# Kernel tuning notes

Measured on AMD Instinct MI355X. Metric: run time of the kernel, lower is better.

The kernel has to match this reference:

```python
import jax, jax.numpy as jnp
import numpy as np

EMBED_DIM = 1024
NUM_HEADS = 16
HEAD_DIM = EMBED_DIM // NUM_HEADS


def setup_inputs() -> dict:
    key = jax.random.key(0)
    k_x, k_wqkv, k_bqkv, k_wout, k_bout = jax.random.split(key, 5)
    scale = 1.0 / np.sqrt(EMBED_DIM)
    return {
        "x": jax.random.normal(k_x, (2, 2048, EMBED_DIM), dtype=jnp.float32),
        "W_qkv": jax.random.normal(k_wqkv, (3 * EMBED_DIM, EMBED_DIM), dtype=jnp.float32) * scale,
        "b_qkv": jax.random.normal(k_bqkv, (3 * EMBED_DIM,), dtype=jnp.float32) * scale,
        "W_out": jax.random.normal(k_wout, (EMBED_DIM, EMBED_DIM), dtype=jnp.float32) * scale,
        "b_out": jax.random.normal(k_bout, (EMBED_DIM,), dtype=jnp.float32) * scale,
    }


def reference(x, W_qkv, b_qkv, W_out, b_out):
    B, L, D = x.shape
    H, hd = NUM_HEADS, HEAD_DIM
    # fused QKV projection (torch Linear: x @ W.T + b)
    qkv = x @ W_qkv.T + b_qkv                      # [B, L, 3D]
    q, k, v = jnp.split(qkv, 3, axis=-1)           # each [B, L, D]
    # [B, L, D] -> [B, H, L, hd]
    q = q.reshape(B, L, H, hd).transpose(0, 2, 1, 3)
    k = k.reshape(B, L, H, hd).transpose(0, 2, 1, 3)
    v = v.reshape(B, L, H, hd).transpose(0, 2, 1, 3)
    attn = jnp.einsum("bhqd,bhkd->bhqk", q, k) / jnp.sqrt(jnp.float32(hd))
    attn = jax.nn.softmax(attn, axis=-1)           # [B, H, L, L]
    out = jnp.einsum("bhqk,bhkd->bhqd", attn, v)   # [B, H, L, hd]
    out = out.transpose(0, 2, 1, 3).reshape(B, L, D)
    return out @ W_out.T + b_out
```

## Files before the change

kernel.cpp:

```cpp
#include <hip/hip_runtime.h>
#include <hip/hip_bf16.h>

typedef __attribute__((ext_vector_type(8))) _Float16 f16x8;
typedef __attribute__((ext_vector_type(4))) _Float16 f16x4;
typedef __attribute__((ext_vector_type(2))) _Float16 f16x2;
typedef __attribute__((ext_vector_type(4))) float f32x4;
typedef __attribute__((ext_vector_type(16))) float f32x16;
typedef __attribute__((ext_vector_type(2))) __fp16 fp16v2;

__device__ __forceinline__ void gload16(const void* g, void* l) {
  __builtin_amdgcn_global_load_lds((const __attribute__((address_space(1))) void*)g,
                                   (__attribute__((address_space(3))) void*)l, 16, 0, 0);
}
__device__ __forceinline__ float fexp2(float x) {
#if __has_builtin(__builtin_amdgcn_exp2f)
  return __builtin_amdgcn_exp2f(x);
#else
  return exp2f(x);
#endif
}
__device__ __forceinline__ unsigned pk2(float a, float b) {
#if __has_builtin(__builtin_amdgcn_cvt_pkrtz)
  fp16v2 r = __builtin_amdgcn_cvt_pkrtz(a, b);
  return __builtin_bit_cast(unsigned, r);
#else
  f16x2 t;
  t[0] = (_Float16)a;
  t[1] = (_Float16)b;
  return __builtin_bit_cast(unsigned, t);
#endif
}

__global__ __launch_bounds__(256) void cast_all(const float* __restrict__ x,
                                                const float* __restrict__ wqkv,
                                                const float* __restrict__ wout,
                                                _Float16* __restrict__ xh,
                                                _Float16* __restrict__ wqkvh,
                                                _Float16* __restrict__ wouth) {
  const int i = (blockIdx.x * 256 + threadIdx.x) * 8;
  const float* s;
  _Float16* d;
  int off;
  if (i < 4194304) {
    s = x; d = xh; off = i;
  } else if (i < 7340032) {
    s = wqkv; d = wqkvh; off = i - 4194304;
  } else {
    s = wout; d = wouth; off = i - 7340032;
  }
  const float4 v0 = *reinterpret_cast<const float4*>(s + off);
  const float4 v1 = *reinterpret_cast<const float4*>(s + off + 4);
  f16x8 h;
  h[0] = (_Float16)v0.x; h[1] = (_Float16)v0.y; h[2] = (_Float16)v0.z; h[3] = (_Float16)v0.w;
  h[4] = (_Float16)v1.x; h[5] = (_Float16)v1.y; h[6] = (_Float16)v1.z; h[7] = (_Float16)v1.w;
  *reinterpret_cast<f16x8*>(d + off) = h;
}

__global__ __launch_bounds__(256) void gemm_qkv(
    const _Float16* __restrict__ A, const _Float16* __restrict__ Bm,
    const float* __restrict__ bias,
    _Float16* __restrict__ Qo, _Float16* __restrict__ Ko, _Float16* __restrict__ Vto,
    int Ndim, int Kdim) {
  __shared__ __align__(16) _Float16 As[2][4096];
  __shared__ __align__(16) _Float16 Bs[2][4096];
  const int tid = threadIdx.x, lane = tid & 63, wave = tid >> 6;
  const int wm = wave >> 1, wn = wave & 1;
  const int nwg = gridDim.x * gridDim.y;
  int bidl = blockIdx.y * gridDim.x + blockIdx.x;
  bidl = (bidl & 7) * (nwg >> 3) + (bidl >> 3);
  const int m0 = (bidl / gridDim.x) * 128, n0 = (bidl % gridDim.x) * 128;
  const int row = lane & 15, kk = (lane >> 4) * 8;

  const int r0 = tid >> 2, c0 = (tid & 3) * 8;
  const int r1 = (256 + tid) >> 2, c1 = ((256 + tid) & 3) * 8;
  const _Float16* a0 = A + (size_t)(m0 + r0) * Kdim + c0;
  const _Float16* a1 = A + (size_t)(m0 + r1) * Kdim + c1;
  const _Float16* b0 = Bm + (size_t)(n0 + r0) * Kdim + c0;
  const _Float16* b1 = Bm + (size_t)(n0 + r1) * Kdim + c1;

  f32x4 acc[4][4];
#pragma unroll
  for (int i = 0; i < 4; ++i)
#pragma unroll
    for (int j = 0; j < 4; ++j)
#pragma unroll
      for (int q = 0; q < 4; ++q) acc[i][j][q] = 0.f;

  auto STAGE = [&](int bufi, int k0) {
    char* dA = (char*)&As[bufi][0] + (wave * 64) * 16;
    char* dB = (char*)&Bs[bufi][0] + (wave * 64) * 16;
    gload16(a0 + k0, dA);
    gload16(a1 + k0, dA + 4096);
    gload16(b0 + k0, dB);
    gload16(b1 + k0, dB + 4096);
  };

  STAGE(0, 0);
  asm volatile("s_waitcnt vmcnt(0)" ::: "memory");
  __syncthreads();

  for (int k0 = 0; k0 < Kdim; k0 += 32) {
    const int cur = (k0 >> 5) & 1;
    if (k0 + 32 < Kdim) STAGE(cur ^ 1, k0 + 32);
    f16x8 af[4], bf[4];
#pragma unroll
    for (int i = 0; i < 4; ++i)
      af[i] = *reinterpret_cast<const f16x8*>(&As[cur][(wm * 64 + i * 16 + row) * 32 + kk]);
#pragma unroll
    for (int j = 0; j < 4; ++j)
      bf[j] = *reinterpret_cast<const f16x8*>(&Bs[cur][(wn * 64 + j * 16 + row) * 32 + kk]);
#pragma unroll
    for (int i = 0; i < 4; ++i)
#pragma unroll
      for (int j = 0; j < 4; ++j)
        acc[i][j] = __builtin_amdgcn_mfma_f32_16x16x32_f16(af[i], bf[j], acc[i][j], 0, 0, 0);
    asm volatile("s_waitcnt vmcnt(0)" ::: "memory");
    __syncthreads();
  }

  const int part = n0 >> 10;
  if (part == 2) {
#pragma unroll
    for (int i = 0; i < 4; ++i) {
      const int gm = m0 + wm * 64 + i * 16 + (lane >> 4) * 4;
      const int b = gm >> 11, l0 = gm & 2047;
#pragma unroll
      for (int j = 0; j < 4; ++j) {
        const int gn = n0 + wn * 64 + j * 16 + row;
        const int dD = gn & 1023;
        const int h = dD >> 6, dd = dD & 63;
        const float bb = bias[gn];
        f16x4 v;
#pragma unroll
        for (int q = 0; q < 4; ++q) v[q] = (_Float16)(acc[i][j][q] + bb);
        *reinterpret_cast<f16x4*>(&Vto[((size_t)(b * 16 + h) * 64 + dd) * 2048 + l0]) = v;
      }
    }
  } else {
#pragma unroll
    for (int i = 0; i < 4; ++i) {
#pragma unroll
      for (int j = 0; j < 4; ++j) {
#pragma unroll
        for (int q = 0; q < 4; ++q) {
          const int gm = m0 + wm * 64 + i * 16 + (lane >> 4) * 4 + q;
          const int gn = n0 + wn * 64 + j * 16 + row;
          const float c = acc[i][j][q] + bias[gn];
          const int b = gm >> 11, l = gm & 2047;
          const int dD = gn & 1023;
          const int h = dD >> 6, dd = dD & 63;
          const int bh = b * 16 + h;
          if (part == 0)
            Qo[((size_t)bh * 2048 + l) * 64 + dd] = (_Float16)(c * 0.1803368801f);
          else
            Ko[((size_t)bh * 2048 + l) * 64 + dd] = (_Float16)c;
        }
      }
    }
  }
}

__global__ __launch_bounds__(256) void gemm_out64(
    const _Float16* __restrict__ A, const _Float16* __restrict__ Bm,
    const float* __restrict__ bias, float* __restrict__ Cout, int Ndim, int Kdim) {
  __shared__ __align__(16) _Float16 As[2][4096];
  __shared__ __align__(16) _Float16 Bs[2][2048];
  const int tid = threadIdx.x, lane = tid & 63, wave = tid >> 6;
  const int wm = wave >> 1, wn = wave & 1;
  const int nwg = gridDim.x * gridDim.y;
  int bidl = blockIdx.y * gridDim.x + blockIdx.x;
  bidl = (bidl & 7) * (nwg >> 3) + (bidl >> 3);
  const int m0 = (bidl / gridDim.x) * 128, n0 = (bidl % gridDim.x) * 64;
  const int row = lane & 15, kk = (lane >> 4) * 8;

  const int r0 = tid >> 2, c0 = (tid & 3) * 8;
  const int r1 = (256 + tid) >> 2, c1 = ((256 + tid) & 3) * 8;
  const _Float16* a0 = A + (size_t)(m0 + r0) * Kdim + c0;
  const _Float16* a1 = A + (size_t)(m0 + r1) * Kdim + c1;
  const _Float16* b0 = Bm + (size_t)(n0 + r0) * Kdim + c0;

  f32x4 acc[4][2];
#pragma unroll
  for (int i = 0; i < 4; ++i)
#pragma unroll
    for (int j = 0; j < 2; ++j)
#pragma unroll
      for (int q = 0; q < 4; ++q) acc[i][j][q] = 0.f;

  auto STAGE = [&](int bufi, int k0) {
    char* dA = (char*)&As[bufi][0] + (wave * 64) * 16;
    char* dB = (char*)&Bs[bufi][0] + wave * 1024;
    gload16(a0 + k0, dA);
    gload16(a1 + k0, dA + 4096);
    gload16(b0 + k0, dB);
  };

  STAGE(0, 0);
  asm volatile("s_waitcnt vmcnt(0)" ::: "memory");
  __syncthreads();

  for (int k0 = 0; k0 < Kdim; k0 += 32) {
    const int cur = (k0 >> 5) & 1;
    if (k0 + 32 < Kdim) STAGE(cur ^ 1, k0 + 32);
    f16x8 af[4], bf[2];
#pragma unroll
    for (int i = 0; i < 4; ++i)
      af[i] = *reinterpret_cast<const f16x8*>(&As[cur][(wm * 64 + i * 16 + row) * 32 + kk]);
#pragma unroll
    for (int j = 0; j < 2; ++j)
      bf[j] = *reinterpret_cast<const f16x8*>(&Bs[cur][(wn * 32 + j * 16 + row) * 32 + kk]);
#pragma unroll
    for (int i = 0; i < 4; ++i)
#pragma unroll
      for (int j = 0; j < 2; ++j)
        acc[i][j] = __builtin_amdgcn_mfma_f32_16x16x32_f16(af[i], bf[j], acc[i][j], 0, 0, 0);
    asm volatile("s_waitcnt vmcnt(0)" ::: "memory");
    __syncthreads();
  }

#pragma unroll
  for (int i = 0; i < 4; ++i) {
#pragma unroll
    for (int j = 0; j < 2; ++j) {
#pragma unroll
      for (int q = 0; q < 4; ++q) {
        const int gm = m0 + wm * 64 + i * 16 + (lane >> 4) * 4 + q;
        const int gn = n0 + wn * 32 + j * 16 + row;
        Cout[(size_t)gm * Ndim + gn] = acc[i][j][q] + bias[gn];
      }
    }
  }
}

__global__ __launch_bounds__(256, 2) void attn_fwd(const _Float16* __restrict__ Qh,
                                                   const _Float16* __restrict__ Kh,
                                                   const _Float16* __restrict__ Vth,
                                                   _Float16* __restrict__ AOh) {
  __shared__ __align__(16) uint4 KVs[2][1024];
  const int tid = threadIdx.x, lane = tid & 63, wave = tid >> 6;
  const int bid = blockIdx.x;
  const int bh = bid & 31, qb = bid >> 5;
  const int b = bh >> 4, h = bh & 15;
  const int q0 = qb * 128 + wave * 32;
  const _Float16* Qp = Qh + ((size_t)bh * 2048 + q0) * 64;
  const _Float16* Kp = Kh + (size_t)bh * 2048 * 64;
  const _Float16* Vp = Vth + (size_t)bh * 64 * 2048;
  const int r31 = lane & 31, hl = lane >> 5, r7 = lane & 7;

  const int kr0 = tid >> 3, ks0 = (tid & 7) ^ (kr0 & 7);
  const int kr1 = (256 + tid) >> 3, ks1 = ((256 + tid) & 7) ^ (kr1 & 7);
  const _Float16* ksrc0 = Kp + (size_t)kr0 * 64 + ks0 * 8;
  const _Float16* ksrc1 = Kp + (size_t)kr1 * 64 + ks1 * 8;
  const _Float16* vsrc0 = Vp + (size_t)kr0 * 2048 + ks0 * 8;
  const _Float16* vsrc1 = Vp + (size_t)kr1 * 2048 + ks1 * 8;

  f16x8 qf[4];
#pragma unroll
  for (int kd = 0; kd < 4; ++kd)
    qf[kd] = *reinterpret_cast<const f16x8*>(&Qp[r31 * 64 + kd * 16 + hl * 8]);

  f32x16 o0, o1;
#pragma unroll
  for (int i = 0; i < 16; ++i) { o0[i] = 0.f; o1[i] = 0.f; }
  float mrun = 0.f, lsum = 0.f;

  auto STAGE = [&](uint4* base, int t) {
    gload16(ksrc0 + (size_t)t * 4096, base + wave * 64);
    gload16(ksrc1 + (size_t)t * 4096, base + 256 + wave * 64);
    gload16(vsrc0 + t * 64, base + 512 + wave * 64);
    gload16(vsrc1 + t * 64, base + 768 + wave * 64);
  };

  auto ITER = [&](int t, uint4* cur, uint4* nxt) {
    if (t < 31) STAGE(nxt, t + 1);
    const char* KB = (const char*)cur;
    const char* VB = (const char*)(cur + 512);

    const float negm = -mrun;
    f32x16 st[2];
    __builtin_amdgcn_s_setprio(1);
#pragma unroll
    for (int t32 = 0; t32 < 2; ++t32) {
#pragma unroll
      for (int i = 0; i < 16; ++i) st[t32][i] = negm;
#pragma unroll
      for (int kd = 0; kd < 4; ++kd) {
        const f16x8 kf = *reinterpret_cast<const f16x8*>(
            KB + (((t32 * 32 + r31) * 8 + ((kd * 2 + hl) ^ r7)) << 4));
        st[t32] = __builtin_amdgcn_mfma_f32_32x32x16_f16(kf, qf[kd], st[t32], 0, 0, 0);
      }
    }
    __builtin_amdgcn_s_setprio(0);

    f16x8 vf[2][2][2];
#pragma unroll
    for (int hh = 0; hh < 2; ++hh)
#pragma unroll
      for (int t32 = 0; t32 < 2; ++t32)
#pragma unroll
        for (int s = 0; s < 2; ++s)
          vf[hh][t32][s] = *reinterpret_cast<const f16x8*>(
              VB + (((hh * 32 + r31) * 8 + (((t32 * 2 + s) * 2 + hl) ^ r7)) << 4));

    float m16[16];
#pragma unroll
    for (int i = 0; i < 16; ++i) m16[i] = fmaxf(st[0][i], st[1][i]);
#pragma unroll
    for (int w = 8; w; w >>= 1)
#pragma unroll
      for (int i = 0; i < 8; ++i)
        if (i < w) m16[i] = fmaxf(m16[i], m16[i + w]);
    const float mt = m16[0];
    if (!__all(mt <= 11.f)) {
      const float mts = fmaxf(mt, __shfl_xor(mt, 32));
      const float d = fmaxf(mts, 0.f);
      const float al = fexp2(-d);
      lsum *= al;
#pragma unroll
      for (int i = 0; i < 16; ++i) { o0[i] *= al; o1[i] *= al; }
      mrun += d;
#pragma unroll
      for (int t32 = 0; t32 < 2; ++t32)
#pragma unroll
        for (int i = 0; i < 16; ++i) st[t32][i] -= d;
    }
    float pr[32];
#pragma unroll
    for (int i = 0; i < 16; ++i) pr[i] = fexp2(st[0][i]);
#pragma unroll
    for (int i = 0; i < 16; ++i) pr[16 + i] = fexp2(st[1][i]);
    float s16[16];
#pragma unroll
    for (int i = 0; i < 16; ++i) s16[i] = pr[i] + pr[16 + i];
#pragma unroll
    for (int w = 8; w; w >>= 1)
#pragma unroll
      for (int i = 0; i < 8; ++i)
        if (i < w) s16[i] += s16[i + w];
    lsum += s16[0];

    __builtin_amdgcn_s_setprio(1);
#pragma unroll
    for (int t32 = 0; t32 < 2; ++t32) {
#pragma unroll
      for (int s = 0; s < 2; ++s) {
        const int bi = t32 * 16 + s * 8;
        const unsigned Aw = pk2(pr[bi + 0], pr[bi + 1]);
        const unsigned A2 = pk2(pr[bi + 2], pr[bi + 3]);
        const unsigned Bw = pk2(pr[bi + 4], pr[bi + 5]);
        const unsigned B2 = pk2(pr[bi + 6], pr[bi + 7]);
        const unsigned r1 = __shfl_xor(hl ? Aw : Bw, 32);
        const unsigned r2 = __shfl_xor(hl ? A2 : B2, 32);
        union { unsigned u[4]; f16x8 v; } pf;
        pf.u[0] = hl ? r1 : Aw;
        pf.u[1] = hl ? r2 : A2;
        pf.u[2] = hl ? Bw : r1;
        pf.u[3] = hl ? B2 : r2;
        o0 = __builtin_amdgcn_mfma_f32_32x32x16_f16(vf[0][t32][s], pf.v, o0, 0, 0, 0);
        o1 = __builtin_amdgcn_mfma_f32_32x32x16_f16(vf[1][t32][s], pf.v, o1, 0, 0, 0);
      }
    }
    __builtin_amdgcn_s_setprio(0);

    if (t < 31) {
      asm volatile("s_waitcnt vmcnt(0)" ::: "memory");
      __syncthreads();
    }
  };

  STAGE(KVs[0], 0);
  asm volatile("s_waitcnt vmcnt(0)" ::: "memory");
  __syncthreads();

  for (int tt = 0; tt < 16; ++tt) {
    ITER(2 * tt, KVs[0], KVs[1]);
    ITER(2 * tt + 1, KVs[1], KVs[0]);
  }

  const float ltot = lsum + __shfl_xor(lsum, 32);
  const float inv = 1.f / ltot;
  const size_t orow = (size_t)b * 2048 + q0 + r31;
#pragma unroll
  for (int hh = 0; hh < 2; ++hh) {
#pragma unroll
    for (int rr = 0; rr < 4; ++rr) {
      f16x4 c;
#pragma unroll
      for (int j = 0; j < 4; ++j)
        c[j] = (_Float16)((hh ? o1[rr * 4 + j] : o0[rr * 4 + j]) * inv);
      const int hd = 8 * rr + 4 * hl + 32 * hh;
      *reinterpret_cast<f16x4*>(&AOh[orow * 1024 + h * 64 + hd]) = c;
    }
  }
}

extern "C" void kernel_launch(void* const* d_in, const int* in_sizes, int n_in, void* d_out,
                              int out_size, void* d_ws, size_t ws_size, hipStream_t stream) {
  const float* x = (const float*)d_in[0];
  const float* Wqkv = (const float*)d_in[1];
  const float* bqkv = (const float*)d_in[2];
  const float* Wout = (const float*)d_in[3];
  const float* bout = (const float*)d_in[4];
  float* out = (float*)d_out;

  char* ws = (char*)d_ws;
  _Float16* xh = (_Float16*)(ws);
  _Float16* wqkvh = (_Float16*)(ws + 8388608);
  _Float16* wouth = (_Float16*)(ws + 14680064);
  _Float16* Qh = (_Float16*)(ws + 16777216);
  _Float16* Kh = (_Float16*)(ws + 25165824);
  _Float16* Vth = (_Float16*)(ws + 33554432);
  _Float16* AOh = (_Float16*)(ws + 41943040);

  cast_all<<<4096, 256, 0, stream>>>(x, Wqkv, Wout, xh, wqkvh, wouth);
  gemm_qkv<<<dim3(24, 32), 256, 0, stream>>>(xh, wqkvh, bqkv, Qh, Kh, Vth, 3072, 1024);
  attn_fwd<<<512, 256, 0, stream>>>(Qh, Kh, Vth, AOh);
  gemm_out64<<<dim3(16, 32), 256, 0, stream>>>(AOh, wouth, bout, out, 1024, 1024);
}
```

Before: 132.1 us.

## Double attention KV tile size to halve barrier count, hoist QK bias loads

The attention kernel now stages 128 keys per shared-memory buffer (two 64-key sub-tiles processed back to back), so the wait-and-barrier step happens 16 times instead of 32, with the V swizzle widened to 16 slots to match. Shared memory per block doubles to 64 KB, which may cut occupancy under the launch bound of 2 blocks. The QK projection epilogue also preloads the four bias values into registers instead of reading bias inside the innermost loop.

```diff
diff --git a/kernel.cpp b/kernel.cpp
--- a/kernel.cpp
+++ b/kernel.cpp
@@ -137,16 +137,19 @@
       }
     }
   } else {
+    float bb[4];
+#pragma unroll
+    for (int j = 0; j < 4; ++j) bb[j] = bias[n0 + wn * 64 + j * 16 + row];
 #pragma unroll
     for (int i = 0; i < 4; ++i) {
 #pragma unroll
-      for (int j = 0; j < 4; ++j) {
-#pragma unroll
-        for (int q = 0; q < 4; ++q) {
-          const int gm = m0 + wm * 64 + i * 16 + (lane >> 4) * 4 + q;
+      for (int q = 0; q < 4; ++q) {
+        const int gm = m0 + wm * 64 + i * 16 + (lane >> 4) * 4 + q;
+        const int b = gm >> 11, l = gm & 2047;
+#pragma unroll
+        for (int j = 0; j < 4; ++j) {
           const int gn = n0 + wn * 64 + j * 16 + row;
-          const float c = acc[i][j][q] + bias[gn];
-          const int b = gm >> 11, l = gm & 2047;
+          const float c = acc[i][j][q] + bb[j];
           const int dD = gn & 1023;
           const int h = dD >> 6, dd = dD & 63;
           const int bh = b * 16 + h;
@@ -236,7 +239,7 @@
                                                    const _Float16* __restrict__ Kh,
                                                    const _Float16* __restrict__ Vth,
                                                    _Float16* __restrict__ AOh) {
-  __shared__ __align__(16) uint4 KVs[2][1024];
+  __shared__ __align__(16) uint4 KVs[2][2048];
   const int tid = threadIdx.x, lane = tid & 63, wave = tid >> 6;
   const int bid = blockIdx.x;
   const int bh = bid & 31, qb = bid >> 5;
@@ -245,14 +248,18 @@
   const _Float16* Qp = Qh + ((size_t)bh * 2048 + q0) * 64;
   const _Float16* Kp = Kh + (size_t)bh * 2048 * 64;
   const _Float16* Vp = Vth + (size_t)bh * 64 * 2048;
-  const int r31 = lane & 31, hl = lane >> 5, r7 = lane & 7;
-
-  const int kr0 = tid >> 3, ks0 = (tid & 7) ^ (kr0 & 7);
-  const int kr1 = (256 + tid) >> 3, ks1 = ((256 + tid) & 7) ^ (kr1 & 7);
-  const _Float16* ksrc0 = Kp + (size_t)kr0 * 64 + ks0 * 8;
-  const _Float16* ksrc1 = Kp + (size_t)kr1 * 64 + ks1 * 8;
-  const _Float16* vsrc0 = Vp + (size_t)kr0 * 2048 + ks0 * 8;
-  const _Float16* vsrc1 = Vp + (size_t)kr1 * 2048 + ks1 * 8;
+  const int r31 = lane & 31, hl = lane >> 5, r7 = lane & 7, r15 = lane & 15;
+
+  const _Float16* ksrcs[4];
+  const _Float16* vsrcs[4];
+#pragma unroll
+  for (int u = 0; u < 4; ++u) {
+    const int gi = u * 256 + tid;
+    const int kr = gi >> 3, ksl = gi & 7;
+    ksrcs[u] = Kp + (size_t)kr * 64 + (ksl ^ (kr & 7)) * 8;
+    const int vr = gi >> 4, vsl = gi & 15;
+    vsrcs[u] = Vp + (size_t)vr * 2048 + (vsl ^ (vr & 15)) * 8;
+  }
 
   f16x8 qf[4];
 #pragma unroll
@@ -265,16 +272,16 @@
   float mrun = 0.f, lsum = 0.f;
 
   auto STAGE = [&](uint4* base, int t) {
-    gload16(ksrc0 + (size_t)t * 4096, base + wave * 64);
-    gload16(ksrc1 + (size_t)t * 4096, base + 256 + wave * 64);
-    gload16(vsrc0 + t * 64, base + 512 + wave * 64);
-    gload16(vsrc1 + t * 64, base + 768 + wave * 64);
+#pragma unroll
+    for (int u = 0; u < 4; ++u) {
+      gload16(ksrcs[u] + (size_t)t * 8192, base + u * 256 + tid);
+      gload16(vsrcs[u] + t * 128, base + 1024 + u * 256 + tid);
+    }
   };
 
-  auto ITER = [&](int t, uint4* cur, uint4* nxt) {
-    if (t < 31) STAGE(nxt, t + 1);
+  auto PROCESS = [&](const uint4* cur, int tt) {
     const char* KB = (const char*)cur;
-    const char* VB = (const char*)(cur + 512);
+    const char* VB = (const char*)(cur + 1024);
 
     const float negm = -mrun;
     f32x16 st[2];
@@ -286,7 +293,7 @@
 #pragma unroll
       for (int kd = 0; kd < 4; ++kd) {
         const f16x8 kf = *reinterpret_cast<const f16x8*>(
-            KB + (((t32 * 32 + r31) * 8 + ((kd * 2 + hl) ^ r7)) << 4));
+            KB + (((tt * 64 + t32 * 32 + r31) * 8 + ((kd * 2 + hl) ^ r7)) << 4));
         st[t32] = __builtin_amdgcn_mfma_f32_32x32x16_f16(kf, qf[kd], st[t32], 0, 0, 0);
       }
     }
@@ -300,7 +307,7 @@
 #pragma unroll
         for (int s = 0; s < 2; ++s)
           vf[hh][t32][s] = *reinterpret_cast<const f16x8*>(
-              VB + (((hh * 32 + r31) * 8 + (((t32 * 2 + s) * 2 + hl) ^ r7)) << 4));
+              VB + (((hh * 32 + r31) * 16 + ((tt * 8 + (t32 * 2 + s) * 2 + hl) ^ r15)) << 4));
 
     float m16[16];
 #pragma unroll
@@ -361,20 +368,21 @@
       }
     }
     __builtin_amdgcn_s_setprio(0);
-
-    if (t < 31) {
-      asm volatile("s_waitcnt vmcnt(0)" ::: "memory");
-      __syncthreads();
-    }
   };
 
   STAGE(KVs[0], 0);
   asm volatile("s_waitcnt vmcnt(0)" ::: "memory");
   __syncthreads();
 
-  for (int tt = 0; tt < 16; ++tt) {
-    ITER(2 * tt, KVs[0], KVs[1]);
-    ITER(2 * tt + 1, KVs[1], KVs[0]);
+  for (int t = 0; t < 16; ++t) {
+    uint4* cur = KVs[t & 1];
+    if (t < 15) STAGE(KVs[(t & 1) ^ 1], t + 1);
+    PROCESS(cur, 0);
+    PROCESS(cur, 1);
+    if (t < 15) {
+      asm volatile("s_waitcnt vmcnt(0)" ::: "memory");
+      __syncthreads();
+    }
   }
 
   const float ltot = lsum + __shfl_xor(lsum, 32);
```

After: 134.6 us. No clear change (+1.9%).
